# Kernel tuning notes

Hardware: AMD Instinct MI355X
Metric: run time of the kernel (lower is better)

Reference implementation:

```python
import jax, jax.numpy as jnp
import numpy as np
from jax import lax

B, C, H, W = 32, 512, 56, 56
CO = 512
EPS = 1e-5

def binarize(x):
    # sign binarization with hardtanh straight-through estimator (BNN 1w1a)
    xc = jnp.clip(x, -1.0, 1.0)
    return xc + lax.stop_gradient(jnp.sign(x) - xc)

def batchnorm(y, g, b, m, v):
    # inference-mode BN with running stats, per-channel over NCHW
    inv = g * lax.rsqrt(v + EPS)
    return y * inv[None, :, None, None] + (b - m * inv)[None, :, None, None]

def setup_inputs() -> dict:
    key = jax.random.key(0)
    ks = jax.random.split(key, 11)
    return {
        "x": jax.random.normal(ks[0], (B, C, H, W), dtype=jnp.float32),
        "w_dw": jax.random.normal(ks[1], (C, 1, 3, 3), dtype=jnp.float32),
        "w_pw": jax.random.normal(ks[2], (CO, C, 1, 1), dtype=jnp.float32),
        "g1": jax.random.uniform(ks[3], (C,), dtype=jnp.float32),
        "b1": jax.random.normal(ks[4], (C,), dtype=jnp.float32),
        "m1": jax.random.normal(ks[5], (C,), dtype=jnp.float32),
        "v1": jax.random.uniform(ks[6], (C,), dtype=jnp.float32),
        "g2": jax.random.uniform(ks[7], (CO,), dtype=jnp.float32),
        "b2": jax.random.normal(ks[8], (CO,), dtype=jnp.float32),
        "m2": jax.random.normal(ks[9], (CO,), dtype=jnp.float32),
        "v2": jax.random.uniform(ks[10], (CO,), dtype=jnp.float32),
    }

def reference(x, w_dw, w_pw, g1, b1, m1, v1, g2, b2, m2, v2):
    dn = ('NCHW', 'OIHW', 'NCHW')
    # binary depthwise 3x3, stride 1, pad 1, groups=C
    out = lax.conv_general_dilated(
        binarize(x), binarize(w_dw), window_strides=(1, 1),
        padding=((1, 1), (1, 1)), feature_group_count=C,
        dimension_numbers=dn)
    out = batchnorm(out, g1, b1, m1, v1)
    # binary pointwise 1x1
    out = lax.conv_general_dilated(
        binarize(out), binarize(w_pw), window_strides=(1, 1),
        padding=((0, 0), (0, 0)), dimension_numbers=dn)
    out = batchnorm(out, g2, b2, m2, v2)
    return out
```

## Files before the change

kernel.cpp:

```cpp
#include <hip/hip_runtime.h>

#define BB 32
#define CC 512
#define COO 512
#define HH 56
#define WW 56
#define HW 3136
#define NPOS 100352
#define EPSF 1e-5f

typedef unsigned long long u64;
typedef unsigned int u32;
typedef unsigned short u16;

#define OFF_S1      0
#define OFF_WBITS   6422528
#define OFF_WN      6455296
#define OFF_NT      6455872
#define OFF_BN2INV  6456832
#define OFF_BN2BETA 6458880

__global__ __launch_bounds__(256) void setup_kernel(
    const float* __restrict__ w_dw, const float* __restrict__ w_pw,
    const float* __restrict__ g1, const float* __restrict__ b1,
    const float* __restrict__ m1, const float* __restrict__ v1,
    const float* __restrict__ g2, const float* __restrict__ b2,
    const float* __restrict__ m2, const float* __restrict__ v2,
    u64* __restrict__ wbits, u64* __restrict__ wn, u64* __restrict__ NT,
    float* __restrict__ bn2inv, float* __restrict__ bn2beta) {
    const int t = blockIdx.x * 256 + threadIdx.x;

    {
        int o = t >> 3, wi = t & 7;
        const float* wp = w_pw + (size_t)o * CC + wi * 64;
        u64 wrd = 0;
        #pragma unroll 8
        for (int k = 0; k < 64; ++k)
            wrd |= (u64)(wp[k] >= 0.f) << k;
        wbits[t] = wrd;
    }

    if (t < CC) {
        float i2 = g2[t] / sqrtf(v2[t] + EPSF);
        bn2inv[t]  = i2;
        bn2beta[t] = b2[t] - m2[t] * i2;
    } else if (t >= 512 && t < 584) {
        int q = t - 512, cw = q & 7, tap = q >> 3;
        u64 wv = 0;
        for (int cl = 0; cl < 64; ++cl)
            wv |= (u64)(w_dw[(size_t)(cw * 64 + cl) * 9 + tap] < 0.f) << cl;
        wn[tap * 8 + cw] = wv;
    } else if (t >= 1024 && t < 1048) {
        int q = t - 1024, cat = q / 8, cw = q % 8;
        const int Nv = (cat == 0) ? 9 : ((cat == 1) ? 6 : 4);
        u64 p0 = 0, p1 = 0, p2 = 0, p3 = 0, F = 0;
        for (int cl = 0; cl < 64; ++cl) {
            int c = cw * 64 + cl;
            float i1 = g1[c] / sqrtf(v1[c] + EPSF);
            float be = b1[c] - m1[c] * i1;
            int T, f;
            if (i1 > 0.f) {
                double h = ((double)Nv - (double)be / (double)i1) * 0.5;
                f = 0;
                if (!(h > 0.0)) T = 0;
                else if (h > 15.0) T = 15;
                else T = (int)ceil(h);
            } else if (i1 < 0.f) {
                double h = ((double)Nv - (double)be / (double)i1) * 0.5;
                f = 1;
                if (h < 0.0) T = 0;
                else if (h >= 15.0) T = 15;
                else { T = (int)floor(h) + 1; if (T > 15) T = 15; }
            } else {
                f = 0;
                T = (be >= 0.f) ? 0 : 15;
            }
            unsigned nt = (~(unsigned)T) & 0xFu;
            p0 |= (u64)(nt & 1) << cl;
            p1 |= (u64)((nt >> 1) & 1) << cl;
            p2 |= (u64)((nt >> 2) & 1) << cl;
            p3 |= (u64)((nt >> 3) & 1) << cl;
            F  |= (u64)f << cl;
        }
        u64* d = NT + (size_t)(cat * 8 + cw) * 5;
        d[0] = p0; d[1] = p1; d[2] = p2; d[3] = p3; d[4] = F;
    }
}

__device__ __forceinline__ void fa(u64 a, u64 b, u64 c, u64& s, u64& cy) {
    u64 ab = a ^ b;
    s  = ab ^ c;
    cy = (ab & c) | (a & b);
}

__global__ __launch_bounds__(512) void dwfused_kernel(
    const float* __restrict__ x, const u64* __restrict__ wn,
    const u64* __restrict__ NT, u64* __restrict__ s1) {
    __shared__ u64 xb[16 * 56];
    const int strip = blockIdx.x;
    const int cw    = blockIdx.y;
    const int b     = blockIdx.z;
    const int tid   = threadIdx.x;
    const int r0    = strip * 14;

    const float* xc = x + ((size_t)b * CC + cw * 64) * HW;
    u16* xb16 = (u16*)xb;

    for (int tau = tid; tau < 896; tau += 512) {
        const int lrow   = tau / 56;
        const int rest   = tau - lrow * 56;
        const int colgrp = rest >> 2, cg = rest & 3;
        const int h      = r0 - 1 + lrow;
        const int col0   = colgrp * 4;
        u16 o0 = 0, o1 = 0, o2 = 0, o3 = 0;
        if (h >= 0 && h < HH) {
            const float* bp = xc + (size_t)(cg * 16) * HW + h * WW + col0;
            u32 a0 = 0, a1 = 0, a2 = 0, a3 = 0;
            #pragma unroll
            for (int cl = 0; cl < 16; ++cl) {
                float4 v = *(const float4*)(bp + (size_t)cl * HW);
                a0 |= (__float_as_uint(v.x) >> 31) << cl;
                a1 |= (__float_as_uint(v.y) >> 31) << cl;
                a2 |= (__float_as_uint(v.z) >> 31) << cl;
                a3 |= (__float_as_uint(v.w) >> 31) << cl;
            }
            o0 = (u16)(~a0); o1 = (u16)(~a1); o2 = (u16)(~a2); o3 = (u16)(~a3);
        }
        const int wbase = lrow * 56 + col0;
        xb16[(wbase + 0) * 4 + cg] = o0;
        xb16[(wbase + 1) * 4 + cg] = o1;
        xb16[(wbase + 2) * 4 + cg] = o2;
        xb16[(wbase + 3) * 4 + cg] = o3;
    }
    __syncthreads();

    const u64 w00 = wn[0*8+cw], w01 = wn[1*8+cw], w02 = wn[2*8+cw];
    const u64 w10 = wn[3*8+cw], w11 = wn[4*8+cw], w12 = wn[5*8+cw];
    const u64 w20 = wn[6*8+cw], w21 = wn[7*8+cw], w22 = wn[8*8+cw];

    for (int task = tid; task < 784; task += 512) {
        const int q = task / 56;
        const int c = task - q * 56;
        const int r = r0 + q;
        const int lrow = q + 1;
        const int cm = (c == 0)  ? 0  : c - 1;
        const int cp = (c == 55) ? 55 : c + 1;

        const u64* rT = xb + (lrow - 1) * 56;
        const u64* rM = xb + lrow * 56;
        const u64* rB = xb + (lrow + 1) * 56;
        u64 t0 = rT[cm], t1 = rT[c], t2 = rT[cp];
        u64 m0 = rM[cm], m1 = rM[c], m2 = rM[cp];
        u64 b0 = rB[cm], b1 = rB[c], b2 = rB[cp];

        const u64 mt = (r > 0)  ? ~0ull : 0ull;
        const u64 mb = (r < 55) ? ~0ull : 0ull;
        const u64 ml = (c > 0)  ? ~0ull : 0ull;
        const u64 mr = (c < 55) ? ~0ull : 0ull;

        u64 e0 = (t0 ^ w00) & mt & ml;
        u64 e1 = (t1 ^ w01) & mt;
        u64 e2 = (t2 ^ w02) & mt & mr;
        u64 e3 = (m0 ^ w10) & ml;
        u64 e4 = (m1 ^ w11);
        u64 e5 = (m2 ^ w12) & mr;
        u64 e6 = (b0 ^ w20) & mb & ml;
        u64 e7 = (b1 ^ w21) & mb;
        u64 e8 = (b2 ^ w22) & mb & mr;

        u64 sa, ca, sb, cb, sc, cc, E0, cd, se, ce;
        fa(e0, e1, e2, sa, ca);
        fa(e3, e4, e5, sb, cb);
        fa(e6, e7, e8, sc, cc);
        fa(sa, sb, sc, E0, cd);
        fa(ca, cb, cc, se, ce);
        u64 E1 = se ^ cd, cf = se & cd;
        u64 E2 = ce ^ cf, E3 = ce & cf;

        const int rowe = (r == 0) | (r == 55);
        const int cole = (c == 0) | (c == 55);
        const u64* NTp = NT + (size_t)(rowe + cole) * 40 + (size_t)cw * 5;
        u64 n0 = NTp[0], n1 = NTp[1], n2 = NTp[2], n3 = NTp[3], Fv = NTp[4];

        u64 cr = E0 | n0;
        cr = (E1 & n1) | (cr & (E1 | n1));
        cr = (E2 & n2) | (cr & (E2 | n2));
        cr = (E3 & n3) | (cr & (E3 | n3));

        s1[(size_t)cw * NPOS + (size_t)b * HW + r * WW + c] = cr ^ Fv;
    }
}

__global__ __launch_bounds__(256) void pw_kernel(
    const u64* __restrict__ s1, const u64* __restrict__ wbits,
    const float* __restrict__ bn2inv, const float* __restrict__ bn2beta,
    float* __restrict__ out) {
    const int tid = threadIdx.x;
    const int o0  = blockIdx.y * 128;

    const size_t p   = (size_t)blockIdx.x * 256 + tid;
    const int    b   = (int)(p / HW);
    const int    idx = (int)(p - (size_t)b * HW);

    u64 r0 = s1[0u * NPOS + p], r1 = s1[1u * NPOS + p];
    u64 r2 = s1[2u * NPOS + p], r3 = s1[3u * NPOS + p];
    u64 r4 = s1[4u * NPOS + p], r5 = s1[5u * NPOS + p];
    u64 r6 = s1[6u * NPOS + p], r7 = s1[7u * NPOS + p];

    const u64*   wp  = wbits + (size_t)o0 * 8;
    const float* ivp = bn2inv + o0;
    const float* btp = bn2beta + o0;
    float* outp = out + ((size_t)b * COO + o0) * HW + idx;

    #pragma unroll 4
    for (int ol = 0; ol < 128; ++ol) {
        const u64* w8 = wp + ol * 8;
        int d = __popcll(r0 ^ w8[0]) + __popcll(r1 ^ w8[1])
              + __popcll(r2 ^ w8[2]) + __popcll(r3 ^ w8[3])
              + __popcll(r4 ^ w8[4]) + __popcll(r5 ^ w8[5])
              + __popcll(r6 ^ w8[6]) + __popcll(r7 ^ w8[7]);
        float res = (float)(CC - 2 * d);
        outp[(size_t)ol * HW] = fmaf(res, ivp[ol], btp[ol]);
    }
}

extern "C" void kernel_launch(void* const* d_in, const int* in_sizes, int n_in,
                              void* d_out, int out_size, void* d_ws, size_t ws_size,
                              hipStream_t stream) {
    const float* x    = (const float*)d_in[0];
    const float* w_dw = (const float*)d_in[1];
    const float* w_pw = (const float*)d_in[2];
    const float* g1   = (const float*)d_in[3];
    const float* b1   = (const float*)d_in[4];
    const float* m1   = (const float*)d_in[5];
    const float* v1   = (const float*)d_in[6];
    const float* g2   = (const float*)d_in[7];
    const float* b2   = (const float*)d_in[8];
    const float* m2   = (const float*)d_in[9];
    const float* v2   = (const float*)d_in[10];

    char* ws = (char*)d_ws;
    u64*   s1      = (u64*)(ws + OFF_S1);
    u64*   wbits   = (u64*)(ws + OFF_WBITS);
    u64*   wn      = (u64*)(ws + OFF_WN);
    u64*   NTarr   = (u64*)(ws + OFF_NT);
    float* bn2inv  = (float*)(ws + OFF_BN2INV);
    float* bn2beta = (float*)(ws + OFF_BN2BETA);

    setup_kernel<<<16, 256, 0, stream>>>(w_dw, w_pw, g1, b1, m1, v1, g2, b2, m2, v2,
                                         wbits, wn, NTarr, bn2inv, bn2beta);

    dim3 gf(4, 8, BB);
    dwfused_kernel<<<gf, 512, 0, stream>>>(x, wn, NTarr, s1);

    dim3 g2d(392, 4);
    pw_kernel<<<g2d, 256, 0, stream>>>(s1, wbits, bn2inv, bn2beta, (float*)d_out);
}
```

Before: 154.4 us.

## Split fused depthwise kernel into separate bit-pack and bitwise conv kernels

Replaces the fused depthwise kernel, which packed x signs into shared memory per 14-row strip (including halo rows) and then ran the 3x3 XNOR-popcount, with two kernels. The first packs the sign bits of the whole input into a global bit buffer, reusing the output buffer as scratch. The second reads 3x3 neighbourhoods straight from that buffer with one thread per position. This removes halo re-reads of the large float input and the low block count of the fused launch (1024 blocks of 512 threads). In exchange it adds a launch and a global round trip for the packed bits, plus 16-bit scattered stores during packing.

```diff
diff --git a/kernel.cpp b/kernel.cpp
--- a/kernel.cpp
+++ b/kernel.cpp
@@ -87,108 +87,98 @@
     }
 }
 
+__global__ __launch_bounds__(256) void xpack_kernel(
+    const float* __restrict__ x, u64* __restrict__ xbits) {
+    const int tau = blockIdx.x * 256 + threadIdx.x;
+    const int cg  = blockIdx.y;
+    const int pg  = tau % 784;
+    const int t2  = tau / 784;
+    const int cw  = t2 & 7, b = t2 >> 3;
+    const int p0  = pg * 4;
+
+    const float* bp = x + ((size_t)b * CC + cw * 64 + cg * 16) * HW + p0;
+    u32 a0 = 0, a1 = 0, a2 = 0, a3 = 0;
+    #pragma unroll
+    for (int cl = 0; cl < 16; ++cl) {
+        float4 v = *(const float4*)(bp + (size_t)cl * HW);
+        a0 |= (__float_as_uint(v.x) >> 31) << cl;
+        a1 |= (__float_as_uint(v.y) >> 31) << cl;
+        a2 |= (__float_as_uint(v.z) >> 31) << cl;
+        a3 |= (__float_as_uint(v.w) >> 31) << cl;
+    }
+    const size_t w = (size_t)cw * NPOS + (size_t)b * HW + p0;
+    u16* sp = (u16*)xbits;
+    sp[(w + 0) * 4 + cg] = (u16)(~a0);
+    sp[(w + 1) * 4 + cg] = (u16)(~a1);
+    sp[(w + 2) * 4 + cg] = (u16)(~a2);
+    sp[(w + 3) * 4 + cg] = (u16)(~a3);
+}
+
 __device__ __forceinline__ void fa(u64 a, u64 b, u64 c, u64& s, u64& cy) {
     u64 ab = a ^ b;
     s  = ab ^ c;
     cy = (ab & c) | (a & b);
 }
 
-__global__ __launch_bounds__(512) void dwfused_kernel(
-    const float* __restrict__ x, const u64* __restrict__ wn,
+__global__ __launch_bounds__(256) void dwbits_kernel(
+    const u64* __restrict__ xbits, const u64* __restrict__ wn,
     const u64* __restrict__ NT, u64* __restrict__ s1) {
-    __shared__ u64 xb[16 * 56];
-    const int strip = blockIdx.x;
-    const int cw    = blockIdx.y;
-    const int b     = blockIdx.z;
-    const int tid   = threadIdx.x;
-    const int r0    = strip * 14;
-
-    const float* xc = x + ((size_t)b * CC + cw * 64) * HW;
-    u16* xb16 = (u16*)xb;
-
-    for (int tau = tid; tau < 896; tau += 512) {
-        const int lrow   = tau / 56;
-        const int rest   = tau - lrow * 56;
-        const int colgrp = rest >> 2, cg = rest & 3;
-        const int h      = r0 - 1 + lrow;
-        const int col0   = colgrp * 4;
-        u16 o0 = 0, o1 = 0, o2 = 0, o3 = 0;
-        if (h >= 0 && h < HH) {
-            const float* bp = xc + (size_t)(cg * 16) * HW + h * WW + col0;
-            u32 a0 = 0, a1 = 0, a2 = 0, a3 = 0;
-            #pragma unroll
-            for (int cl = 0; cl < 16; ++cl) {
-                float4 v = *(const float4*)(bp + (size_t)cl * HW);
-                a0 |= (__float_as_uint(v.x) >> 31) << cl;
-                a1 |= (__float_as_uint(v.y) >> 31) << cl;
-                a2 |= (__float_as_uint(v.z) >> 31) << cl;
-                a3 |= (__float_as_uint(v.w) >> 31) << cl;
-            }
-            o0 = (u16)(~a0); o1 = (u16)(~a1); o2 = (u16)(~a2); o3 = (u16)(~a3);
-        }
-        const int wbase = lrow * 56 + col0;
-        xb16[(wbase + 0) * 4 + cg] = o0;
-        xb16[(wbase + 1) * 4 + cg] = o1;
-        xb16[(wbase + 2) * 4 + cg] = o2;
-        xb16[(wbase + 3) * 4 + cg] = o3;
-    }
-    __syncthreads();
+    const int cw = blockIdx.y;
+    const size_t p = (size_t)blockIdx.x * 256 + threadIdx.x;
+    const int b   = (int)(p / HW);
+    const int idx = (int)(p - (size_t)b * HW);
+    const int r   = idx / WW;
+    const int c   = idx - r * WW;
+
+    const u64* xp = xbits + (size_t)cw * NPOS + (size_t)b * HW;
+    const int rm = (r == 0)  ? 0  : r - 1;
+    const int rp = (r == 55) ? 55 : r + 1;
+    const int cm = (c == 0)  ? 0  : c - 1;
+    const int cp = (c == 55) ? 55 : c + 1;
+
+    u64 t0 = xp[rm * WW + cm], t1 = xp[rm * WW + c], t2 = xp[rm * WW + cp];
+    u64 m0 = xp[r  * WW + cm], m1 = xp[r  * WW + c], m2 = xp[r  * WW + cp];
+    u64 b0 = xp[rp * WW + cm], b1 = xp[rp * WW + c], b2 = xp[rp * WW + cp];
 
     const u64 w00 = wn[0*8+cw], w01 = wn[1*8+cw], w02 = wn[2*8+cw];
     const u64 w10 = wn[3*8+cw], w11 = wn[4*8+cw], w12 = wn[5*8+cw];
     const u64 w20 = wn[6*8+cw], w21 = wn[7*8+cw], w22 = wn[8*8+cw];
 
-    for (int task = tid; task < 784; task += 512) {
-        const int q = task / 56;
-        const int c = task - q * 56;
-        const int r = r0 + q;
-        const int lrow = q + 1;
-        const int cm = (c == 0)  ? 0  : c - 1;
-        const int cp = (c == 55) ? 55 : c + 1;
-
-        const u64* rT = xb + (lrow - 1) * 56;
-        const u64* rM = xb + lrow * 56;
-        const u64* rB = xb + (lrow + 1) * 56;
-        u64 t0 = rT[cm], t1 = rT[c], t2 = rT[cp];
-        u64 m0 = rM[cm], m1 = rM[c], m2 = rM[cp];
-        u64 b0 = rB[cm], b1 = rB[c], b2 = rB[cp];
-
-        const u64 mt = (r > 0)  ? ~0ull : 0ull;
-        const u64 mb = (r < 55) ? ~0ull : 0ull;
-        const u64 ml = (c > 0)  ? ~0ull : 0ull;
-        const u64 mr = (c < 55) ? ~0ull : 0ull;
-
-        u64 e0 = (t0 ^ w00) & mt & ml;
-        u64 e1 = (t1 ^ w01) & mt;
-        u64 e2 = (t2 ^ w02) & mt & mr;
-        u64 e3 = (m0 ^ w10) & ml;
-        u64 e4 = (m1 ^ w11);
-        u64 e5 = (m2 ^ w12) & mr;
-        u64 e6 = (b0 ^ w20) & mb & ml;
-        u64 e7 = (b1 ^ w21) & mb;
-        u64 e8 = (b2 ^ w22) & mb & mr;
-
-        u64 sa, ca, sb, cb, sc, cc, E0, cd, se, ce;
-        fa(e0, e1, e2, sa, ca);
-        fa(e3, e4, e5, sb, cb);
-        fa(e6, e7, e8, sc, cc);
-        fa(sa, sb, sc, E0, cd);
-        fa(ca, cb, cc, se, ce);
-        u64 E1 = se ^ cd, cf = se & cd;
-        u64 E2 = ce ^ cf, E3 = ce & cf;
-
-        const int rowe = (r == 0) | (r == 55);
-        const int cole = (c == 0) | (c == 55);
-        const u64* NTp = NT + (size_t)(rowe + cole) * 40 + (size_t)cw * 5;
-        u64 n0 = NTp[0], n1 = NTp[1], n2 = NTp[2], n3 = NTp[3], Fv = NTp[4];
-
-        u64 cr = E0 | n0;
-        cr = (E1 & n1) | (cr & (E1 | n1));
-        cr = (E2 & n2) | (cr & (E2 | n2));
-        cr = (E3 & n3) | (cr & (E3 | n3));
-
-        s1[(size_t)cw * NPOS + (size_t)b * HW + r * WW + c] = cr ^ Fv;
-    }
+    const u64 mt = (r > 0)  ? ~0ull : 0ull;
+    const u64 mb = (r < 55) ? ~0ull : 0ull;
+    const u64 ml = (c > 0)  ? ~0ull : 0ull;
+    const u64 mr = (c < 55) ? ~0ull : 0ull;
+
+    u64 e0 = (t0 ^ w00) & mt & ml;
+    u64 e1 = (t1 ^ w01) & mt;
+    u64 e2 = (t2 ^ w02) & mt & mr;
+    u64 e3 = (m0 ^ w10) & ml;
+    u64 e4 = (m1 ^ w11);
+    u64 e5 = (m2 ^ w12) & mr;
+    u64 e6 = (b0 ^ w20) & mb & ml;
+    u64 e7 = (b1 ^ w21) & mb;
+    u64 e8 = (b2 ^ w22) & mb & mr;
+
+    u64 sa, ca, sb, cb, sc, cc, E0, cd, se, ce;
+    fa(e0, e1, e2, sa, ca);
+    fa(e3, e4, e5, sb, cb);
+    fa(e6, e7, e8, sc, cc);
+    fa(sa, sb, sc, E0, cd);
+    fa(ca, cb, cc, se, ce);
+    u64 E1 = se ^ cd, cf = se & cd;
+    u64 E2 = ce ^ cf, E3 = ce & cf;
+
+    const int rowe = (r == 0) | (r == 55);
+    const int cole = (c == 0) | (c == 55);
+    const u64* NTp = NT + (size_t)(rowe + cole) * 40 + (size_t)cw * 5;
+    u64 n0 = NTp[0], n1 = NTp[1], n2 = NTp[2], n3 = NTp[3], Fv = NTp[4];
+
+    u64 cr = E0 | n0;
+    cr = (E1 & n1) | (cr & (E1 | n1));
+    cr = (E2 & n2) | (cr & (E2 | n2));
+    cr = (E3 & n3) | (cr & (E3 | n3));
+
+    s1[(size_t)cw * NPOS + p] = cr ^ Fv;
 }
 
 __global__ __launch_bounds__(256) void pw_kernel(
@@ -246,12 +236,16 @@
     u64*   NTarr   = (u64*)(ws + OFF_NT);
     float* bn2inv  = (float*)(ws + OFF_BN2INV);
     float* bn2beta = (float*)(ws + OFF_BN2BETA);
+    u64*   xbits   = (u64*)d_out;
 
     setup_kernel<<<16, 256, 0, stream>>>(w_dw, w_pw, g1, b1, m1, v1, g2, b2, m2, v2,
                                          wbits, wn, NTarr, bn2inv, bn2beta);
 
-    dim3 gf(4, 8, BB);
-    dwfused_kernel<<<gf, 512, 0, stream>>>(x, wn, NTarr, s1);
+    dim3 g0(784, 4);
+    xpack_kernel<<<g0, 256, 0, stream>>>(x, xbits);
+
+    dim3 g1d(392, 8);
+    dwbits_kernel<<<g1d, 256, 0, stream>>>(xbits, wn, NTarr, s1);
 
     dim3 g2d(392, 4);
     pw_kernel<<<g2d, 256, 0, stream>>>(s1, wbits, bn2inv, bn2beta, (float*)d_out);
```

Result: slower. 164.3 us (+6.4%).
